# Performance work log

Hardware: AMD Instinct MI355X
Metric: run time of the kernel (lower is better)

Reference implementation:

```python
import jax, jax.numpy as jnp
import numpy as np

BOND_D = 4    # disentangler bond dim (hard-coded 4 in torch init)
BOND_I = 16   # isometry bond dim (bond_dim kwarg)
F = 2         # feature_dim = 2*nCh, nCh=1 -> [x, 1-x] embedding
LEVELS = [128, 64, 32, 16, 8, 4]
NUM_CLASSES = 10
BATCH = 16


def setup_inputs() -> dict:
    key = jax.random.key(0)
    ks = iter(jax.random.split(key, 128))
    inp = {}
    inp["x"] = jax.random.uniform(next(ks), (BATCH, 1, 128, 128), dtype=jnp.float32)

    def mps_params(P, D, O):
        A = 0.2 * jax.random.normal(next(ks), (P, 4, F, D, D), dtype=jnp.float32)
        v = 0.2 * jax.random.normal(next(ks), (P, D), dtype=jnp.float32)
        w = 0.2 * jax.random.normal(next(ks), (P, D, O), dtype=jnp.float32)
        return A, v, w

    for l, H in enumerate(LEVELS, start=1):
        Pd = ((H - 2) // 2) ** 2   # number of disentangler patches
        Pi = (H // 2) ** 2         # number of isometry patches
        inp[f"d{l}A"], inp[f"d{l}v"], inp[f"d{l}w"] = mps_params(Pd, BOND_D, 4)
        inp[f"i{l}A"], inp[f"i{l}v"], inp[f"i{l}w"] = mps_params(Pi, BOND_I, 1)
    inp["fA"], inp["fv"], inp["fw"] = mps_params(1, BOND_I, NUM_CLASSES)
    return inp


def _patches(x):
    # x: [b, H, W] (H, W even) -> [b, (H/2)*(W/2), 4], same site order as
    # torch unfold(2,2,2).unfold(3,2,2).reshape(..., 4)
    b, H, W = x.shape
    return x.reshape(b, H // 2, 2, W // 2, 2).transpose(0, 1, 3, 2, 4).reshape(b, -1, 4)


def _unpatch(y, nh, nw):
    # y: [b, nh*nw, 4] -> [b, 2*nh, 2*nw], inverse spatial placement of 2x2 blocks
    b = y.shape[0]
    return y.reshape(b, nh, nw, 2, 2).transpose(0, 1, 3, 2, 4).reshape(b, 2 * nh, 2 * nw)


def _mps(patches, A, v, w):
    # Batched per-patch ReLU-MPS over 4 sites.
    # patches [b,P,4], A [P,4,F,D,D], v [P,D], w [P,D,O] -> [b,P,O]
    phi = jnp.stack([patches, 1.0 - patches], axis=-1)          # [b,P,4,F]
    M = jnp.einsum('bpsf,psfij->bpsij', phi, A)                 # [b,P,4,D,D]
    vec = jnp.einsum('pi,bpij->bpj', v, M[:, :, 0])             # [b,P,D]
    for s in range(1, 4):
        vec = jnp.einsum('bpi,bpij->bpj', vec, M[:, :, s])
    return jax.nn.relu(jnp.einsum('bpi,pio->bpo', vec, w))


def _level(x, dA, dv, dw, iA, iv, iw):
    # One MERA layer: disentangle shifted interior patches, write back, then
    # isometry-pool the full grid 2x2 -> 1.
    b, H, W = x.shape
    nh = (H - 2) // 2
    y = _mps(_patches(x[:, 1:-1, 1:-1]), dA, dv, dw)            # [b, nh*nh, 4]
    x = x.at[:, 1:-1, 1:-1].set(_unpatch(y, nh, nh))
    y2 = _mps(_patches(x), iA, iv, iw)                          # [b, (H/2)^2, 1]
    return y2.reshape(b, H // 2, W // 2)


def reference(x, d1A, d1v, d1w, i1A, i1v, i1w,
              d2A, d2v, d2w, i2A, i2v, i2w,
              d3A, d3v, d3w, i3A, i3v, i3w,
              d4A, d4v, d4w, i4A, i4v, i4w,
              d5A, d5v, d5w, i5A, i5v, i5w,
              d6A, d6v, d6w, i6A, i6v, i6w,
              fA, fv, fw):
    h = x[:, 0]  # nCh = 1
    levels = [(d1A, d1v, d1w, i1A, i1v, i1w), (d2A, d2v, d2w, i2A, i2v, i2w),
              (d3A, d3v, d3w, i3A, i3v, i3w), (d4A, d4v, d4w, i4A, i4v, i4w),
              (d5A, d5v, d5w, i5A, i5v, i5w), (d6A, d6v, d6w, i6A, i6v, i6w)]
    for p in levels:
        h = _level(h, *p)
    flat = h.reshape(h.shape[0], 1, 4)         # final 2x2 grid -> 4 sites
    return _mps(flat, fA, fv, fw)[:, 0]        # [b, NUM_CLASSES]
```

## Files before the change

kernel.cpp:

```cpp
#include <hip/hip_runtime.h>

#define BATCH 16

__global__ __launch_bounds__(256) void d_kernel_j(
    float* __restrict__ h, const float* __restrict__ A,
    const float* __restrict__ v, const float* __restrict__ w,
    int H, int nh) {
  int g = blockIdx.x * blockDim.x + threadIdx.x;
  int total = nh * nh * BATCH * 4;
  if (g >= total) return;
  int j = g & 3;
  int b = (g >> 2) & 15;
  int p = g >> 6;
  int pi = p / nh, pj = p % nh;
  float* xb = h + (size_t)b * H * H;
  int r0 = 1 + 2 * pi, c0 = 1 + 2 * pj;
  float t[4];
  t[0] = xb[r0 * H + c0];
  t[1] = xb[r0 * H + c0 + 1];
  t[2] = xb[(r0 + 1) * H + c0];
  t[3] = xb[(r0 + 1) * H + c0 + 1];
  const float* Ap = A + (size_t)p * 128;
  float vec = v[p * 4 + j];
#pragma unroll
  for (int s = 0; s < 4; s++) {
    float ts = t[s], us = 1.0f - ts;
    const float* A0 = Ap + s * 32;
    const float* A1 = A0 + 16;
    float vn = 0.0f;
#pragma unroll
    for (int i = 0; i < 4; i++) {
      float m = ts * A0[i * 4 + j] + us * A1[i * 4 + j];
      vn += __shfl(vec, i, 4) * m;
    }
    vec = vn;
  }
  float acc = 0.0f;
#pragma unroll
  for (int i = 0; i < 4; i++) acc += __shfl(vec, i, 4) * w[p * 16 + i * 4 + j];
  acc = fmaxf(acc, 0.0f);
  int r = r0 + (j >> 1), c = c0 + (j & 1);
  xb[r * H + c] = acc;
}

__global__ __launch_bounds__(256) void i_kernel_j(
    const float* __restrict__ h, float* __restrict__ hn,
    const float* __restrict__ A, const float* __restrict__ v,
    const float* __restrict__ w, int H) {
  int W2 = H >> 1;
  int g = blockIdx.x * blockDim.x + threadIdx.x;
  int j = g & 15;
  int b = (g >> 4) & 15;
  int p = g >> 8;
  int pi = p / W2, pj = p % W2;
  const float* xb = h + (size_t)b * H * H;
  int r0 = 2 * pi, c0 = 2 * pj;
  float t[4];
  t[0] = xb[r0 * H + c0];
  t[1] = xb[r0 * H + c0 + 1];
  t[2] = xb[(r0 + 1) * H + c0];
  t[3] = xb[(r0 + 1) * H + c0 + 1];
  const float* Ap = A + (size_t)p * 2048;
  float vec = v[p * 16 + j];
#pragma unroll
  for (int s = 0; s < 4; s++) {
    float ts = t[s], us = 1.0f - ts;
    const float* A0 = Ap + s * 512;
    const float* A1 = A0 + 256;
    float vn = 0.0f;
#pragma unroll
    for (int i = 0; i < 16; i++) {
      float m = ts * A0[i * 16 + j] + us * A1[i * 16 + j];
      vn += __shfl(vec, i, 16) * m;
    }
    vec = vn;
  }
  float partial = vec * w[p * 16 + j];
#pragma unroll
  for (int off = 8; off >= 1; off >>= 1)
    partial += __shfl_xor(partial, off, 16);
  if (j == 0) hn[(size_t)b * W2 * W2 + p] = fmaxf(partial, 0.0f);
}

__global__ void final_kernel(const float* __restrict__ h6,
                             const float* __restrict__ A,
                             const float* __restrict__ v,
                             const float* __restrict__ w,
                             float* __restrict__ out) {
  int b = threadIdx.x;
  if (b >= BATCH) return;
  float t[4];
#pragma unroll
  for (int s = 0; s < 4; s++) t[s] = h6[b * 4 + s];
  float vec[16];
#pragma unroll
  for (int i = 0; i < 16; i++) vec[i] = v[i];
#pragma unroll
  for (int s = 0; s < 4; s++) {
    float ts = t[s], us = 1.0f - ts;
    const float* A0 = A + s * 512;
    const float* A1 = A0 + 256;
    float vn[16];
#pragma unroll
    for (int q = 0; q < 16; q++) vn[q] = 0.0f;
#pragma unroll
    for (int i = 0; i < 16; i++) {
      float vi = vec[i];
#pragma unroll
      for (int q = 0; q < 16; q++)
        vn[q] += vi * (ts * A0[i * 16 + q] + us * A1[i * 16 + q]);
    }
#pragma unroll
    for (int q = 0; q < 16; q++) vec[q] = vn[q];
  }
#pragma unroll
  for (int o = 0; o < 10; o++) {
    float acc = 0.f;
#pragma unroll
    for (int i = 0; i < 16; i++) acc += vec[i] * w[i * 10 + o];
    out[b * 10 + o] = fmaxf(acc, 0.0f);
  }
}

extern "C" void kernel_launch(void* const* d_in, const int* in_sizes, int n_in,
                              void* d_out, int out_size, void* d_ws, size_t ws_size,
                              hipStream_t stream) {
  const float* x = (const float*)d_in[0];
  float* ws = (float*)d_ws;

  hipMemcpyAsync(ws, x, (size_t)BATCH * 128 * 128 * sizeof(float),
                 hipMemcpyDeviceToDevice, stream);

  int H = 128;
  size_t hoff = 0;
  for (int l = 0; l < 6; l++) {
    const float* dA = (const float*)d_in[1 + 6 * l + 0];
    const float* dv = (const float*)d_in[1 + 6 * l + 1];
    const float* dw = (const float*)d_in[1 + 6 * l + 2];
    const float* iA = (const float*)d_in[1 + 6 * l + 3];
    const float* iv = (const float*)d_in[1 + 6 * l + 4];
    const float* iw = (const float*)d_in[1 + 6 * l + 5];

    int nh = (H - 2) / 2;
    int totd = nh * nh * BATCH * 4;
    d_kernel_j<<<(totd + 255) / 256, 256, 0, stream>>>(ws + hoff, dA, dv, dw, H, nh);

    int W2 = H / 2;
    size_t hoff_next = hoff + (size_t)BATCH * H * H;
    int toti = W2 * W2 * BATCH * 16;
    i_kernel_j<<<toti / 256, 256, 0, stream>>>(ws + hoff, ws + hoff_next,
                                               iA, iv, iw, H);
    hoff = hoff_next;
    H = W2;
  }

  final_kernel<<<1, 64, 0, stream>>>(ws + hoff, (const float*)d_in[37],
                                     (const float*)d_in[38],
                                     (const float*)d_in[39], (float*)d_out);
}
```

Before: 230.2 us.

## Fuse disentangler into isometry per level and collapse small levels into one kernel

Each level now runs as a single kernel in which every 4-lane group recomputes the disentangler output for its isometry input cell directly, instead of writing back into a copied buffer. The initial device-to-device memcpy goes away, and levels 4-6 plus the final MPS are merged into one per-batch block kernel that keeps intermediates in shared memory. Together these cut the launch count from 14 to 4 and remove global round trips. In exchange, each disentangler patch is evaluated redundantly by several isometry groups, adding compute and redundant parameter loads.

```diff
diff --git a/kernel.cpp b/kernel.cpp
--- a/kernel.cpp
+++ b/kernel.cpp
@@ -2,123 +2,156 @@
 
 #define BATCH 16
 
-__global__ __launch_bounds__(256) void d_kernel_j(
-    float* __restrict__ h, const float* __restrict__ A,
-    const float* __restrict__ v, const float* __restrict__ w,
-    int H, int nh) {
-  int g = blockIdx.x * blockDim.x + threadIdx.x;
-  int total = nh * nh * BATCH * 4;
-  if (g >= total) return;
-  int j = g & 3;
-  int b = (g >> 2) & 15;
-  int p = g >> 6;
-  int pi = p / nh, pj = p % nh;
-  float* xb = h + (size_t)b * H * H;
-  int r0 = 1 + 2 * pi, c0 = 1 + 2 * pj;
+template <int H>
+__device__ __forceinline__ float fused_di_unit(
+    const float* __restrict__ xb,
+    int p, int j,
+    const float* __restrict__ dA, const float* __restrict__ dv,
+    const float* __restrict__ dw,
+    const float* __restrict__ iA, const float* __restrict__ iv,
+    const float* __restrict__ iw) {
+  constexpr int NH = (H - 2) / 2;
+  constexpr int W2 = H / 2;
+  int pi = p / W2, pj = p % W2;
+  int sg = j >> 2, j4 = j & 3;
+  int r = 2 * pi + (sg >> 1), c = 2 * pj + (sg & 1);
+  float tcell;
+  bool border = (r == 0) | (r == H - 1) | (c == 0) | (c == H - 1);
+  if (border) {
+    tcell = xb[r * H + c];
+  } else {
+    int dpi = (r - 1) >> 1, dpj = (c - 1) >> 1;
+    int sd = ((r - 1) & 1) * 2 + ((c - 1) & 1);
+    int dp = dpi * NH + dpj;
+    int R0 = 1 + 2 * dpi, C0 = 1 + 2 * dpj;
+    float tin = xb[(R0 + (j4 >> 1)) * H + (C0 + (j4 & 1))];
+    const float* Ap = dA + dp * 128;
+    float vec = dv[dp * 4 + j4];
+#pragma unroll
+    for (int s = 0; s < 4; s++) {
+      float ts = __shfl(tin, s, 4);
+      const float* A0 = Ap + s * 32;
+      float q0 = 0.f, q1 = 0.f;
+#pragma unroll
+      for (int i = 0; i < 4; i++) {
+        float sv = __shfl(vec, i, 4);
+        q0 = fmaf(sv, A0[i * 4 + j4], q0);
+        q1 = fmaf(sv, A0[16 + i * 4 + j4], q1);
+      }
+      vec = ts * q0 + (1.0f - ts) * q1;
+    }
+    float y = 0.f;
+#pragma unroll
+    for (int i = 0; i < 4; i++)
+      y = fmaf(__shfl(vec, i, 4), dw[dp * 16 + i * 4 + j4], y);
+    y = fmaxf(y, 0.0f);
+    tcell = __shfl(y, sd, 4);
+  }
   float t[4];
-  t[0] = xb[r0 * H + c0];
-  t[1] = xb[r0 * H + c0 + 1];
-  t[2] = xb[(r0 + 1) * H + c0];
-  t[3] = xb[(r0 + 1) * H + c0 + 1];
-  const float* Ap = A + (size_t)p * 128;
-  float vec = v[p * 4 + j];
+  t[0] = __shfl(tcell, 0, 16);
+  t[1] = __shfl(tcell, 4, 16);
+  t[2] = __shfl(tcell, 8, 16);
+  t[3] = __shfl(tcell, 12, 16);
+  const float* Ap = iA + p * 2048;
+  float vec = iv[p * 16 + j];
 #pragma unroll
   for (int s = 0; s < 4; s++) {
-    float ts = t[s], us = 1.0f - ts;
-    const float* A0 = Ap + s * 32;
-    const float* A1 = A0 + 16;
-    float vn = 0.0f;
+    const float* A0 = Ap + s * 512;
+    float q0 = 0.f, q1 = 0.f;
 #pragma unroll
-    for (int i = 0; i < 4; i++) {
-      float m = ts * A0[i * 4 + j] + us * A1[i * 4 + j];
-      vn += __shfl(vec, i, 4) * m;
+    for (int i = 0; i < 16; i++) {
+      float sv = __shfl(vec, i, 16);
+      q0 = fmaf(sv, A0[i * 16 + j], q0);
+      q1 = fmaf(sv, A0[256 + i * 16 + j], q1);
     }
-    vec = vn;
+    vec = t[s] * q0 + (1.0f - t[s]) * q1;
   }
-  float acc = 0.0f;
+  float partial = vec * iw[p * 16 + j];
 #pragma unroll
-  for (int i = 0; i < 4; i++) acc += __shfl(vec, i, 4) * w[p * 16 + i * 4 + j];
-  acc = fmaxf(acc, 0.0f);
-  int r = r0 + (j >> 1), c = c0 + (j & 1);
-  xb[r * H + c] = acc;
+  for (int off = 8; off >= 1; off >>= 1)
+    partial += __shfl_xor(partial, off, 16);
+  return fmaxf(partial, 0.0f);
 }
 
-__global__ __launch_bounds__(256) void i_kernel_j(
-    const float* __restrict__ h, float* __restrict__ hn,
-    const float* __restrict__ A, const float* __restrict__ v,
-    const float* __restrict__ w, int H) {
-  int W2 = H >> 1;
-  int g = blockIdx.x * blockDim.x + threadIdx.x;
+template <int H>
+__global__ __launch_bounds__(256) void level_kernel(
+    const float* __restrict__ xin, float* __restrict__ hn,
+    const float* __restrict__ dA, const float* __restrict__ dv,
+    const float* __restrict__ dw, const float* __restrict__ iA,
+    const float* __restrict__ iv, const float* __restrict__ iw) {
+  constexpr int W2 = H / 2;
+  int g = blockIdx.x * 256 + threadIdx.x;
   int j = g & 15;
   int b = (g >> 4) & 15;
   int p = g >> 8;
-  int pi = p / W2, pj = p % W2;
-  const float* xb = h + (size_t)b * H * H;
-  int r0 = 2 * pi, c0 = 2 * pj;
-  float t[4];
-  t[0] = xb[r0 * H + c0];
-  t[1] = xb[r0 * H + c0 + 1];
-  t[2] = xb[(r0 + 1) * H + c0];
-  t[3] = xb[(r0 + 1) * H + c0 + 1];
-  const float* Ap = A + (size_t)p * 2048;
-  float vec = v[p * 16 + j];
+  const float* xb = xin + b * H * H;
+  float o = fused_di_unit<H>(xb, p, j, dA, dv, dw, iA, iv, iw);
+  if (j == 0) hn[b * W2 * W2 + p] = o;
+}
+
+struct TailArgs {
+  const float* h3;
+  const float* in[21];
+  float* out;
+};
+
+__global__ __launch_bounds__(1024) void tail_kernel(TailArgs a) {
+  __shared__ float x4[256];
+  __shared__ float h4[64];
+  __shared__ float h5[16];
+  __shared__ float h6[4];
+  int b = blockIdx.x;
+  int tid = threadIdx.x;
+  if (tid < 256) x4[tid] = a.h3[b * 256 + tid];
+  __syncthreads();
+  {
+    int j = tid & 15, p = tid >> 4;
+    float o = fused_di_unit<16>(x4, p, j, a.in[0], a.in[1], a.in[2],
+                                a.in[3], a.in[4], a.in[5]);
+    if (j == 0) h4[p] = o;
+  }
+  __syncthreads();
+  if (tid < 256) {
+    int j = tid & 15, p = tid >> 4;
+    float o = fused_di_unit<8>(h4, p, j, a.in[6], a.in[7], a.in[8],
+                               a.in[9], a.in[10], a.in[11]);
+    if (j == 0) h5[p] = o;
+  }
+  __syncthreads();
+  if (tid < 64) {
+    int j = tid & 15, p = tid >> 4;
+    float o = fused_di_unit<4>(h5, p, j, a.in[12], a.in[13], a.in[14],
+                               a.in[15], a.in[16], a.in[17]);
+    if (j == 0) h6[p] = o;
+  }
+  __syncthreads();
+  if (tid < 16) {
+    int j = tid;
+    const float* fA = a.in[18];
+    const float* fv = a.in[19];
+    const float* fw = a.in[20];
+    float t[4] = {h6[0], h6[1], h6[2], h6[3]};
+    float vec = fv[j];
 #pragma unroll
-  for (int s = 0; s < 4; s++) {
-    float ts = t[s], us = 1.0f - ts;
-    const float* A0 = Ap + s * 512;
-    const float* A1 = A0 + 256;
-    float vn = 0.0f;
+    for (int s = 0; s < 4; s++) {
+      const float* A0 = fA + s * 512;
+      float q0 = 0.f, q1 = 0.f;
+#pragma unroll
+      for (int i = 0; i < 16; i++) {
+        float sv = __shfl(vec, i, 16);
+        q0 = fmaf(sv, A0[i * 16 + j], q0);
+        q1 = fmaf(sv, A0[256 + i * 16 + j], q1);
+      }
+      vec = t[s] * q0 + (1.0f - t[s]) * q1;
+    }
+    float acc = 0.0f;
 #pragma unroll
     for (int i = 0; i < 16; i++) {
-      float m = ts * A0[i * 16 + j] + us * A1[i * 16 + j];
-      vn += __shfl(vec, i, 16) * m;
+      float sv = __shfl(vec, i, 16);
+      float wv = (j < 10) ? fw[i * 10 + j] : 0.0f;
+      acc = fmaf(sv, wv, acc);
     }
-    vec = vn;
-  }
-  float partial = vec * w[p * 16 + j];
-#pragma unroll
-  for (int off = 8; off >= 1; off >>= 1)
-    partial += __shfl_xor(partial, off, 16);
-  if (j == 0) hn[(size_t)b * W2 * W2 + p] = fmaxf(partial, 0.0f);
-}
-
-__global__ void final_kernel(const float* __restrict__ h6,
-                             const float* __restrict__ A,
-                             const float* __restrict__ v,
-                             const float* __restrict__ w,
-                             float* __restrict__ out) {
-  int b = threadIdx.x;
-  if (b >= BATCH) return;
-  float t[4];
-#pragma unroll
-  for (int s = 0; s < 4; s++) t[s] = h6[b * 4 + s];
-  float vec[16];
-#pragma unroll
-  for (int i = 0; i < 16; i++) vec[i] = v[i];
-#pragma unroll
-  for (int s = 0; s < 4; s++) {
-    float ts = t[s], us = 1.0f - ts;
-    const float* A0 = A + s * 512;
-    const float* A1 = A0 + 256;
-    float vn[16];
-#pragma unroll
-    for (int q = 0; q < 16; q++) vn[q] = 0.0f;
-#pragma unroll
-    for (int i = 0; i < 16; i++) {
-      float vi = vec[i];
-#pragma unroll
-      for (int q = 0; q < 16; q++)
-        vn[q] += vi * (ts * A0[i * 16 + q] + us * A1[i * 16 + q]);
-    }
-#pragma unroll
-    for (int q = 0; q < 16; q++) vec[q] = vn[q];
-  }
-#pragma unroll
-  for (int o = 0; o < 10; o++) {
-    float acc = 0.f;
-#pragma unroll
-    for (int i = 0; i < 16; i++) acc += vec[i] * w[i * 10 + o];
-    out[b * 10 + o] = fmaxf(acc, 0.0f);
+    if (j < 10) a.out[b * 10 + j] = fmaxf(acc, 0.0f);
   }
 }
 
@@ -127,34 +160,26 @@
                               hipStream_t stream) {
   const float* x = (const float*)d_in[0];
   float* ws = (float*)d_ws;
+  float* h1 = ws;
+  float* h2 = h1 + 65536;
+  float* h3 = h2 + 16384;
 
-  hipMemcpyAsync(ws, x, (size_t)BATCH * 128 * 128 * sizeof(float),
-                 hipMemcpyDeviceToDevice, stream);
+  level_kernel<128><<<64 * 64, 256, 0, stream>>>(
+      x, h1, (const float*)d_in[1], (const float*)d_in[2],
+      (const float*)d_in[3], (const float*)d_in[4], (const float*)d_in[5],
+      (const float*)d_in[6]);
+  level_kernel<64><<<32 * 32, 256, 0, stream>>>(
+      h1, h2, (const float*)d_in[7], (const float*)d_in[8],
+      (const float*)d_in[9], (const float*)d_in[10], (const float*)d_in[11],
+      (const float*)d_in[12]);
+  level_kernel<32><<<16 * 16, 256, 0, stream>>>(
+      h2, h3, (const float*)d_in[13], (const float*)d_in[14],
+      (const float*)d_in[15], (const float*)d_in[16], (const float*)d_in[17],
+      (const float*)d_in[18]);
 
-  int H = 128;
-  size_t hoff = 0;
-  for (int l = 0; l < 6; l++) {
-    const float* dA = (const float*)d_in[1 + 6 * l + 0];
-    const float* dv = (const float*)d_in[1 + 6 * l + 1];
-    const float* dw = (const float*)d_in[1 + 6 * l + 2];
-    const float* iA = (const float*)d_in[1 + 6 * l + 3];
-    const float* iv = (const float*)d_in[1 + 6 * l + 4];
-    const float* iw = (const float*)d_in[1 + 6 * l + 5];
-
-    int nh = (H - 2) / 2;
-    int totd = nh * nh * BATCH * 4;
-    d_kernel_j<<<(totd + 255) / 256, 256, 0, stream>>>(ws + hoff, dA, dv, dw, H, nh);
-
-    int W2 = H / 2;
-    size_t hoff_next = hoff + (size_t)BATCH * H * H;
-    int toti = W2 * W2 * BATCH * 16;
-    i_kernel_j<<<toti / 256, 256, 0, stream>>>(ws + hoff, ws + hoff_next,
-                                               iA, iv, iw, H);
-    hoff = hoff_next;
-    H = W2;
-  }
-
-  final_kernel<<<1, 64, 0, stream>>>(ws + hoff, (const float*)d_in[37],
-                                     (const float*)d_in[38],
-                                     (const float*)d_in[39], (float*)d_out);
+  TailArgs ta;
+  ta.h3 = h3;
+  for (int i = 0; i < 21; i++) ta.in[i] = (const float*)d_in[19 + i];
+  ta.out = (float*)d_out;
+  tail_kernel<<<BATCH, 1024, 0, stream>>>(ta);
 }
```

Measured after the change: 216.8 us. 5.8% less time.
